# Kernel optimization log

Hardware: AMD Instinct MI355X
Metric: run time of the kernel (lower is better)

## Reference

```python
import jax, jax.numpy as jnp
import numpy as np

B, S, E, H = 4, 2048, 1024, 16
D = E // H  # per-head dim = 64


def setup_inputs() -> dict:
    key = jax.random.key(0)
    k1, k2, k3 = jax.random.split(key, 3)
    x = jax.random.normal(k1, (B, S, E), dtype=jnp.float32)
    # per-head nn.Linear(d, 3d, bias=False) weights, torch layout [3d, d]
    W_qkv = jax.random.normal(k2, (H, 3 * D, D), dtype=jnp.float32) * (D ** -0.5)
    # output projection nn.Linear(E, E, bias=False), torch layout [E, E]
    W_out = jax.random.normal(k3, (E, E), dtype=jnp.float32) * (E ** -0.5)
    return {"x": x, "W_qkv": W_qkv, "W_out": W_out}


def reference(x, W_qkv, W_out):
    b, s, e = x.shape
    h, td, d = W_qkv.shape  # td = 3*d
    # chunk along embedding dim -> [b, s, h, d]
    xh = x.reshape(b, s, h, d)
    # per-head linear: y = x @ W.T ; qkv layout from torch view(..., 3, d):
    # first d outputs are q, next d are k, last d are v
    qkv = jnp.einsum('bshd,hed->bshe', xh, W_qkv)  # [b, s, h, 3d]
    qkv = qkv.reshape(b, s, h, 3, d)
    q = qkv[..., 0, :].transpose(0, 2, 1, 3)  # [b, h, s, d]
    k = qkv[..., 1, :].transpose(0, 2, 1, 3)
    v = qkv[..., 2, :].transpose(0, 2, 1, 3)
    scores = jnp.einsum('bhid,bhjd->bhij', q, k) * (d ** -0.5)
    attn = jax.nn.softmax(scores, axis=-1)
    out = jnp.einsum('bhij,bhjd->bhid', attn, v)  # [b, h, s, d]
    out = out.transpose(0, 2, 1, 3).reshape(b, s, e)
    return out @ W_out.T
```

## Files before the change

kernel.cpp:

```cpp
#include <hip/hip_runtime.h>
#include <hip/hip_bf16.h>

#define NBATCH 4
#define NS 2048
#define NE 1024
#define NH 16
#define ND 64

typedef __attribute__((ext_vector_type(4))) float f32x4;
typedef __attribute__((ext_vector_type(16))) float f32x16;
typedef __attribute__((ext_vector_type(8))) short s16x8;
typedef __attribute__((ext_vector_type(2))) unsigned u32x2;

__device__ __forceinline__ unsigned short f2bf(float f) {
  union { float f; unsigned u; } v; v.f = f;
  return (unsigned short)((v.u + 0x7fffu + ((v.u >> 16) & 1u)) >> 16);
}

__device__ __forceinline__ unsigned cvt_pk_bf16(float lo, float hi) {
  unsigned r;
  asm("v_cvt_pk_bf16_f32 %0, %1, %2" : "=v"(r) : "v"(lo), "v"(hi));
  return r;
}

typedef const __attribute__((address_space(1))) void* gas_t;
typedef __attribute__((address_space(3))) void* las_t;

__global__ __launch_bounds__(256) void cvt_kernel(
    const float* __restrict__ wqkv, const float* __restrict__ wout,
    unsigned short* __restrict__ wqb, unsigned short* __restrict__ wob) {
  const int NQ = NH * 3 * ND * ND / 4, NO = NE * NE / 4;
  const int total = NQ + NO;
  for (int i = blockIdx.x * blockDim.x + threadIdx.x; i < total;
       i += gridDim.x * blockDim.x) {
    const float4* s; unsigned short* d; int j;
    if (i < NQ) { s = (const float4*)wqkv; d = wqb; j = i; }
    else        { s = (const float4*)wout; d = wob; j = i - NQ; }
    float4 v = s[j];
    ushort4 o;
    o.x = f2bf(v.x); o.y = f2bf(v.y); o.z = f2bf(v.z); o.w = f2bf(v.w);
    ((ushort4*)d)[j] = o;
  }
}

__global__ __launch_bounds__(256) void qkv_kernel(
    const float* __restrict__ x, const unsigned short* __restrict__ wqb,
    unsigned short* __restrict__ Qb, unsigned short* __restrict__ Kb,
    unsigned short* __restrict__ Vt) {
  int blk = blockIdx.x;
  int st = blk & 31;
  int bh = blk >> 5;
  int h = bh & 15;
  int b = bh >> 4;
  int tid = threadIdx.x, w = tid >> 6, l = tid & 63, lm = l & 15, lg = l >> 4;
  int s0 = st * 64 + w * 16;

  const float* xrow = x + (size_t)(b * NS + s0 + lm) * NE + h * ND;
  float4 f0 = *(const float4*)(xrow + lg * 8);
  float4 f1 = *(const float4*)(xrow + lg * 8 + 4);
  float4 f2 = *(const float4*)(xrow + 32 + lg * 8);
  float4 f3 = *(const float4*)(xrow + 32 + lg * 8 + 4);
  union { unsigned u[4]; s16x8 v; } A0, A1;
  A0.u[0] = cvt_pk_bf16(f0.x, f0.y); A0.u[1] = cvt_pk_bf16(f0.z, f0.w);
  A0.u[2] = cvt_pk_bf16(f1.x, f1.y); A0.u[3] = cvt_pk_bf16(f1.z, f1.w);
  A1.u[0] = cvt_pk_bf16(f2.x, f2.y); A1.u[1] = cvt_pk_bf16(f2.z, f2.w);
  A1.u[2] = cvt_pk_bf16(f3.x, f3.y); A1.u[3] = cvt_pk_bf16(f3.z, f3.w);
  s16x8 a0 = A0.v, a1 = A1.v;

  const unsigned short* wb = wqb + h * 3 * ND * ND;
  size_t bhS = (size_t)bh * NS;
  const float QSCALE = 0.125f * 1.44269504089f;

#pragma unroll
  for (int nb = 0; nb < 12; nb++) {
    f32x4 acc = (f32x4){0.f, 0.f, 0.f, 0.f};
    const unsigned short* wr_ = wb + (nb * 16 + lm) * ND + lg * 8;
    acc = __builtin_amdgcn_mfma_f32_16x16x32_bf16(a0, *(const s16x8*)wr_, acc, 0, 0, 0);
    acc = __builtin_amdgcn_mfma_f32_16x16x32_bf16(a1, *(const s16x8*)(wr_ + 32), acc, 0, 0, 0);
    int e = nb * 16 + lm;
    if (nb < 4) {
#pragma unroll
      for (int r = 0; r < 4; r++)
        Qb[(bhS + s0 + lg * 4 + r) * ND + e] = f2bf(acc[r] * QSCALE);
    } else if (nb < 8) {
#pragma unroll
      for (int r = 0; r < 4; r++)
        Kb[(bhS + s0 + lg * 4 + r) * ND + (e - 64)] = f2bf(acc[r]);
    } else {
#pragma unroll
      for (int r = 0; r < 4; r++)
        Vt[((size_t)bh * ND + (e - 128)) * NS + s0 + lg * 4 + r] = f2bf(acc[r]);
    }
  }
}


#define STAGE(bufsel)                                                          \
  {                                                                            \
    unsigned short* lp = smem + (bufsel) * 8192 + w * 2048;                    \
    _Pragma("unroll")                                                          \
    for (int i = 0; i < 4; i++)                                                \
      __builtin_amdgcn_global_load_lds((gas_t)(gsrc + i * istep),              \
                                       (las_t)(lp + i * 512), 16, 0, 0);       \
    gsrc += gstep;                                                             \
  }

#define COMPUTE(BUFBASE)                                                       \
  {                                                                            \
    const char* kb_ = BUFBASE;                                                 \
    s16x8 k0[4], k1[4];                                                        \
    _Pragma("unroll")                                                          \
    for (int dk = 0; dk < 4; dk++) {                                           \
      k0[dk] = *(const s16x8*)(kb_ + off0[dk]);                                \
      k1[dk] = *(const s16x8*)(kb_ + off0[dk] + 4096);                         \
    }                                                                          \
    f32x16 s0, s1;                                                             \
    s0 = __builtin_amdgcn_mfma_f32_32x32x16_bf16(k0[0], qf[0], zero16, 0, 0, 0);\
    s1 = __builtin_amdgcn_mfma_f32_32x32x16_bf16(k1[0], qf[0], zero16, 0, 0, 0);\
    _Pragma("unroll")                                                          \
    for (int dk = 1; dk < 4; dk++) {                                           \
      s0 = __builtin_amdgcn_mfma_f32_32x32x16_bf16(k0[dk], qf[dk], s0, 0, 0, 0);\
      s1 = __builtin_amdgcn_mfma_f32_32x32x16_bf16(k1[dk], qf[dk], s1, 0, 0, 0);\
    }                                                                          \
    s16x8 vf0[4], vf1[4];                                                      \
    _Pragma("unroll")                                                          \
    for (int ks = 0; ks < 4; ks++) {                                           \
      vf0[ks] = *(const s16x8*)(kb_ + off0[ks] + 8192);                        \
      vf1[ks] = *(const s16x8*)(kb_ + off0[ks] + 12288);                       \
    }                                                                          \
    _Pragma("unroll")                                                          \
    for (int r = 0; r < 16; r++) {                                             \
      s0[r] = __builtin_amdgcn_exp2f(s0[r]);                                   \
      s1[r] = __builtin_amdgcn_exp2f(s1[r]);                                   \
    }                                                                          \
           \
    s16x8 pa[4];                                                               \
    _Pragma("unroll")                                                          \
    for (int ks = 0; ks < 4; ks++) {                                           \
      const f32x16& pt = (ks >= 2) ? s1 : s0;                                  \
      const int R = (ks & 1) * 8;                                              \
      unsigned a0 = cvt_pk_bf16(pt[R + 0], pt[R + 1]);                         \
      unsigned a1 = cvt_pk_bf16(pt[R + 2], pt[R + 3]);                         \
      unsigned b0 = cvt_pk_bf16(pt[R + 4], pt[R + 5]);                         \
      unsigned b1 = cvt_pk_bf16(pt[R + 6], pt[R + 7]);                         \
      u32x2 r0 = __builtin_amdgcn_permlane32_swap(a0, b0, false, false);       \
      u32x2 r1 = __builtin_amdgcn_permlane32_swap(a1, b1, false, false);       \
      union { unsigned u[4]; s16x8 v; } fr;                                    \
      fr.u[0] = r0[0]; fr.u[1] = r1[0]; fr.u[2] = r0[1]; fr.u[3] = r1[1];      \
      pa[ks] = fr.v;                                                           \
    }                                                                          \
                                       \
    _Pragma("unroll")                                                          \
    for (int ks = 0; ks < 4; ks++) {                                           \
      o0 = __builtin_amdgcn_mfma_f32_32x32x16_bf16(vf0[ks], pa[ks], o0, 0, 0, 0);\
      o1 = __builtin_amdgcn_mfma_f32_32x32x16_bf16(vf1[ks], pa[ks], o1, 0, 0, 0);\
      accl = __builtin_amdgcn_mfma_f32_32x32x16_bf16(ones, pa[ks], accl, 0, 0, 0);\
    }                                                                          \
  }

__global__ __launch_bounds__(256) void attn_kernel(
    const unsigned short* __restrict__ Qb, const unsigned short* __restrict__ Kb,
    const unsigned short* __restrict__ Vt, unsigned short* __restrict__ AOb) {
  __shared__ __align__(16) unsigned short smem[16384];
  int blk = blockIdx.x;
  int wg = (blk & 7) * 128 + (blk >> 3);
  int qt = wg & 15;
  int bh = wg >> 4;
  int h = bh & 15;
  int b = bh >> 4;
  int tid = threadIdx.x, w = tid >> 6, l = tid & 63, c = l & 31, hi = l >> 5;
  int q0 = qt * 128 + w * 32;

  const unsigned short* Qh = Qb + (size_t)bh * NS * ND;
  const unsigned short* Kh = Kb + (size_t)bh * NS * ND;
  const unsigned short* Vh = Vt + (size_t)bh * ND * NS;

  int lrow = (w & 1) * 32 + (l >> 3);
  int chg = (l & 7) ^ (l >> 3);
  const unsigned short* gsrc;
  size_t istep, gstep;
  if (w < 2) { gsrc = Kh + (size_t)lrow * ND + chg * 8;  istep = 8 * ND;   gstep = 64 * ND; }
  else       { gsrc = Vh + (size_t)lrow * NS + chg * 8;  istep = 8 * NS;   gstep = 64; }

  int off0[4];
#pragma unroll
  for (int dk = 0; dk < 4; dk++)
    off0[dk] = c * 128 + (((dk * 2 + hi) ^ (c & 7)) * 16);

  s16x8 qf[4];
#pragma unroll
  for (int dk = 0; dk < 4; dk++)
    qf[dk] = *(const s16x8*)(Qh + (size_t)(q0 + c) * ND + dk * 16 + hi * 8);

  union { unsigned u[4]; s16x8 v; } onesu;
  onesu.u[0] = onesu.u[1] = onesu.u[2] = onesu.u[3] = 0x3F803F80u;
  s16x8 ones = onesu.v;

  f32x16 o0, o1, accl, zero16;
#pragma unroll
  for (int r = 0; r < 16; r++) { o0[r] = 0.f; o1[r] = 0.f; accl[r] = 0.f; zero16[r] = 0.f; }

  STAGE(0);
  __syncthreads();

  int cur = 0;
  for (int t = 0; t < 32; t++) {
    if (t < 31) STAGE(cur ^ 1);
    COMPUTE((const char*)smem + cur * 16384);
    __syncthreads();
    cur ^= 1;
  }

  float inv = 1.0f / accl[0];
  unsigned short* pl = smem + w * 2176;
#pragma unroll
  for (int dt = 0; dt < 2; dt++) {
#pragma unroll
    for (int rg = 0; rg < 4; rg++) {
      float v0 = (dt ? o1[rg * 4 + 0] : o0[rg * 4 + 0]) * inv;
      float v1 = (dt ? o1[rg * 4 + 1] : o0[rg * 4 + 1]) * inv;
      float v2 = (dt ? o1[rg * 4 + 2] : o0[rg * 4 + 2]) * inv;
      float v3 = (dt ? o1[rg * 4 + 3] : o0[rg * 4 + 3]) * inv;
      uint2 val;
      val.x = cvt_pk_bf16(v0, v1);
      val.y = cvt_pk_bf16(v2, v3);
      int dbase = dt * 32 + rg * 8 + 4 * hi;
      *reinterpret_cast<uint2*>(pl + c * 68 + dbase) = val;
    }
  }
  asm volatile("s_waitcnt lgkmcnt(0)" ::: "memory");
#pragma unroll
  for (int p = 0; p < 4; p++) {
    int row = p * 8 + (l >> 3);
    int co = (l & 7) * 8;
    uint2 x0 = *reinterpret_cast<const uint2*>(pl + row * 68 + co);
    uint2 x1 = *reinterpret_cast<const uint2*>(pl + row * 68 + co + 4);
    uint4 val; val.x = x0.x; val.y = x0.y; val.z = x1.x; val.w = x1.y;
    *reinterpret_cast<uint4*>(AOb + ((size_t)(b * NS + q0 + row)) * NE + h * ND + co) = val;
  }
}


#define STAGEP(BUF, koff)                                                      \
  {                                                                            \
    unsigned short* la = &smem[(BUF)][w * 512];                                \
    unsigned short* lb = &smem[(BUF)][8192 + w * 512];                         \
    _Pragma("unroll")                                                          \
    for (int i = 0; i < 4; i++) {                                              \
      __builtin_amdgcn_global_load_lds((gas_t)(gA + (size_t)i * 32 * NE + (koff)),\
                                       (las_t)(la + i * 2048), 16, 0, 0);      \
      __builtin_amdgcn_global_load_lds((gas_t)(gB + (size_t)i * 32 * NE + (koff)),\
                                       (las_t)(lb + i * 2048), 16, 0, 0);      \
    }                                                                          \
  }

__global__ __launch_bounds__(256) void proj_kernel(
    const unsigned short* __restrict__ A, const unsigned short* __restrict__ Bw,
    float* __restrict__ C) {
  __shared__ __align__(16) unsigned short smem[2][16384];
  int blk = blockIdx.x;
  int xcd = blk & 7, idx = blk >> 3;
  int bm = xcd * 8 + (idx >> 3);
  int bn = idx & 7;
  int tid = threadIdx.x, w = tid >> 6, l = tid & 63, c = l & 31, hi = l >> 5;
  int wr = w >> 1, wc = w & 1;
  int m0 = bm * 128, n0 = bn * 128;

  int srow = tid >> 3;
  int g = (tid & 7) ^ ((tid >> 3) & 7);
  const unsigned short* gA = A + (size_t)(m0 + srow) * NE + g * 8;
  const unsigned short* gB = Bw + (size_t)(n0 + srow) * NE + g * 8;

  int offA[2][4], offB[2][4];
#pragma unroll
  for (int mt = 0; mt < 2; mt++)
#pragma unroll
    for (int ks = 0; ks < 4; ks++) {
      offA[mt][ks] = (wr * 64 + mt * 32 + c) * 128 + (((ks * 2 + hi) ^ (c & 7)) * 16);
      offB[mt][ks] = (wc * 64 + mt * 32 + c) * 128 + (((ks * 2 + hi) ^ (c & 7)) * 16);
    }

  f32x16 a00, a01, a10, a11;
#pragma unroll
  for (int r = 0; r < 16; r++) { a00[r] = 0.f; a01[r] = 0.f; a10[r] = 0.f; a11[r] = 0.f; }

  STAGEP(0, 0);
  __syncthreads();

  int cur = 0;
  for (int t = 0; t < 16; t++) {
    if (t < 15) STAGEP(cur ^ 1, (t + 1) * 64);
    {
      const char* ab = (const char*)&smem[cur][0];
      const char* bb = (const char*)&smem[cur][8192];
#pragma unroll
      for (int ks = 0; ks < 4; ks++) {
        s16x8 fa0 = *(const s16x8*)(ab + offA[0][ks]);
        s16x8 fa1 = *(const s16x8*)(ab + offA[1][ks]);
        s16x8 fb0 = *(const s16x8*)(bb + offB[0][ks]);
        s16x8 fb1 = *(const s16x8*)(bb + offB[1][ks]);
        a00 = __builtin_amdgcn_mfma_f32_32x32x16_bf16(fa0, fb0, a00, 0, 0, 0);
        a01 = __builtin_amdgcn_mfma_f32_32x32x16_bf16(fa0, fb1, a01, 0, 0, 0);
        a10 = __builtin_amdgcn_mfma_f32_32x32x16_bf16(fa1, fb0, a10, 0, 0, 0);
        a11 = __builtin_amdgcn_mfma_f32_32x32x16_bf16(fa1, fb1, a11, 0, 0, 0);
      }
    }
    __syncthreads();
    cur ^= 1;
  }

#pragma unroll
  for (int mt = 0; mt < 2; mt++)
#pragma unroll
    for (int nt = 0; nt < 2; nt++) {
      const f32x16& acc = mt == 0 ? (nt == 0 ? a00 : a01) : (nt == 0 ? a10 : a11);
#pragma unroll
      for (int r = 0; r < 16; r++) {
        int mrow = m0 + wr * 64 + mt * 32 + (r & 3) + 8 * (r >> 2) + 4 * hi;
        int ncol = n0 + wc * 64 + nt * 32 + c;
        C[(size_t)mrow * NE + ncol] = acc[r];
      }
    }
}

extern "C" void kernel_launch(void* const* d_in, const int* in_sizes, int n_in,
                              void* d_out, int out_size, void* d_ws, size_t ws_size,
                              hipStream_t stream) {
  const float* x    = (const float*)d_in[0];
  const float* wqkv = (const float*)d_in[1];
  const float* wout = (const float*)d_in[2];
  float* out = (float*)d_out;
  char* ws = (char*)d_ws;

  size_t off = 0;
  unsigned short* wqb = (unsigned short*)(ws + off); off += (size_t)NH * 3 * ND * ND * 2;
  unsigned short* wob = (unsigned short*)(ws + off); off += (size_t)NE * NE * 2;
  unsigned short* Qb  = (unsigned short*)(ws + off); off += (size_t)NBATCH * NH * NS * ND * 2;
  unsigned short* Kb  = (unsigned short*)(ws + off); off += (size_t)NBATCH * NH * NS * ND * 2;
  unsigned short* Vt  = (unsigned short*)(ws + off); off += (size_t)NBATCH * NH * NS * ND * 2;
  unsigned short* AOb = (unsigned short*)(ws + off); off += (size_t)NBATCH * NS * NE * 2;

  cvt_kernel<<<1024, 256, 0, stream>>>(wqkv, wout, wqb, wob);
  qkv_kernel<<<2048, 256, 0, stream>>>(x, wqb, Qb, Kb, Vt);
  attn_kernel<<<1024, 256, 0, stream>>>(Qb, Kb, Vt, AOb);
  proj_kernel<<<512, 256, 0, stream>>>(AOb, wob, out);
}
```

Before: 150.3 us.

## Triple-buffer K/V LDS staging with vmcnt-based barriers and MFMA priority boosts

Replaces the double-buffered K/V staging with a three-buffer rotation. The prefetch runs two tiles ahead, and each iteration uses an explicit s_waitcnt vmcnt(4) plus a single s_barrier instead of a full __syncthreads after compute. The goal is to hide global-to-LDS load latency and drop one barrier per iteration. It also raises wave priority around the MFMA blocks so the matrix pipes stay fed. LDS use grows from 32KB to 48KB per block, which could lower occupancy, and the barrier correctness depends on the vmcnt accounting.

```diff
diff --git a/kernel.cpp b/kernel.cpp
--- a/kernel.cpp
+++ b/kernel.cpp
@@ -95,9 +95,9 @@
 }
 
 
-#define STAGE(bufsel)                                                          \
+#define STAGE_TO(BUFP)                                                         \
   {                                                                            \
-    unsigned short* lp = smem + (bufsel) * 8192 + w * 2048;                    \
+    unsigned short* lp = (BUFP) + w * 2048;                                    \
     _Pragma("unroll")                                                          \
     for (int i = 0; i < 4; i++)                                                \
       __builtin_amdgcn_global_load_lds((gas_t)(gsrc + i * istep),              \
@@ -107,7 +107,7 @@
 
 #define COMPUTE(BUFBASE)                                                       \
   {                                                                            \
-    const char* kb_ = BUFBASE;                                                 \
+    const char* kb_ = (const char*)(BUFBASE);                                  \
     s16x8 k0[4], k1[4];                                                        \
     _Pragma("unroll")                                                          \
     for (int dk = 0; dk < 4; dk++) {                                           \
@@ -115,6 +115,7 @@
       k1[dk] = *(const s16x8*)(kb_ + off0[dk] + 4096);                         \
     }                                                                          \
     f32x16 s0, s1;                                                             \
+    __builtin_amdgcn_s_setprio(1);                                             \
     s0 = __builtin_amdgcn_mfma_f32_32x32x16_bf16(k0[0], qf[0], zero16, 0, 0, 0);\
     s1 = __builtin_amdgcn_mfma_f32_32x32x16_bf16(k1[0], qf[0], zero16, 0, 0, 0);\
     _Pragma("unroll")                                                          \
@@ -122,6 +123,7 @@
       s0 = __builtin_amdgcn_mfma_f32_32x32x16_bf16(k0[dk], qf[dk], s0, 0, 0, 0);\
       s1 = __builtin_amdgcn_mfma_f32_32x32x16_bf16(k1[dk], qf[dk], s1, 0, 0, 0);\
     }                                                                          \
+    __builtin_amdgcn_s_setprio(0);                                             \
     s16x8 vf0[4], vf1[4];                                                      \
     _Pragma("unroll")                                                          \
     for (int ks = 0; ks < 4; ks++) {                                           \
@@ -150,18 +152,26 @@
       pa[ks] = fr.v;                                                           \
     }                                                                          \
                                        \
+    __builtin_amdgcn_s_setprio(1);                                             \
     _Pragma("unroll")                                                          \
     for (int ks = 0; ks < 4; ks++) {                                           \
       o0 = __builtin_amdgcn_mfma_f32_32x32x16_bf16(vf0[ks], pa[ks], o0, 0, 0, 0);\
       o1 = __builtin_amdgcn_mfma_f32_32x32x16_bf16(vf1[ks], pa[ks], o1, 0, 0, 0);\
       accl = __builtin_amdgcn_mfma_f32_32x32x16_bf16(ones, pa[ks], accl, 0, 0, 0);\
     }                                                                          \
-  }
+    __builtin_amdgcn_s_setprio(0);                                             \
+  }
+
+#define WAIT_BARRIER(N)                                                        \
+  asm volatile("s_waitcnt vmcnt(" #N ")" ::: "memory");                        \
+  __builtin_amdgcn_sched_barrier(0);                                           \
+  __builtin_amdgcn_s_barrier();                                                \
+  __builtin_amdgcn_sched_barrier(0);
 
 __global__ __launch_bounds__(256) void attn_kernel(
     const unsigned short* __restrict__ Qb, const unsigned short* __restrict__ Kb,
     const unsigned short* __restrict__ Vt, unsigned short* __restrict__ AOb) {
-  __shared__ __align__(16) unsigned short smem[16384];
+  __shared__ __align__(16) unsigned short smem[24576];
   int blk = blockIdx.x;
   int wg = (blk & 7) * 128 + (blk >> 3);
   int qt = wg & 15;
@@ -200,16 +210,22 @@
 #pragma unroll
   for (int r = 0; r < 16; r++) { o0[r] = 0.f; o1[r] = 0.f; accl[r] = 0.f; zero16[r] = 0.f; }
 
-  STAGE(0);
-  __syncthreads();
-
-  int cur = 0;
-  for (int t = 0; t < 32; t++) {
-    if (t < 31) STAGE(cur ^ 1);
-    COMPUTE((const char*)smem + cur * 16384);
-    __syncthreads();
-    cur ^= 1;
-  }
+  unsigned short* cA = smem;
+  unsigned short* cB = smem + 8192;
+  unsigned short* cC = smem + 16384;
+
+  STAGE_TO(cA);
+  STAGE_TO(cB);
+
+  for (int t = 0; t < 31; t++) {
+    WAIT_BARRIER(4);
+    if (t < 30) STAGE_TO(cC);
+    COMPUTE(cA);
+    unsigned short* tmp = cA; cA = cB; cB = cC; cC = tmp;
+  }
+  WAIT_BARRIER(0);
+  COMPUTE(cA);
+  __builtin_amdgcn_s_barrier();
 
   float inv = 1.0f / accl[0];
   unsigned short* pl = smem + w * 2176;
```

Result: slower. 160.1 us (+6.5%).
